# Performance work log

Measured on AMD Instinct MI355X. Metric: run time of the kernel, lower is better.

Reference implementation:

```python
import jax, jax.numpy as jnp
import numpy as np

EMBED_DIM = 256
MIN_SCALE = 0.5
BASE = 100.0
NDIM = 3
EPS = 1e-5


def basis_norm(psi, w):
    # w: [B, N] float weights; reduce over token dim (-2)
    norm_sq = jnp.sum(w[..., None] * (psi * psi), axis=-2, keepdims=True)
    return psi / jnp.sqrt(norm_sq + EPS)


def rotary(f, coords, lift):
    # lift: [D//2, 3]; phase: [B, N, D//2]
    phase = coords @ lift.T
    c, s = jnp.cos(phase), jnp.sin(phase)
    f1, f2 = jnp.split(f, 2, axis=-1)
    return jnp.concatenate([f1 * c - f2 * s, f1 * s + f2 * c], axis=-1)


def setup_inputs() -> dict:
    key = jax.random.key(0)
    ks = jax.random.split(key, 12)
    B, N, D = 4, 8192, EMBED_DIM
    phi = jax.random.normal(ks[0], (B, N, D), dtype=jnp.float32)
    coords = jax.random.normal(ks[1], (B, N, NDIM), dtype=jnp.float32)
    weights = jax.random.uniform(ks[2], (B, N), dtype=jnp.float32)
    scale = 1.0 / np.sqrt(D)
    Wq = jax.random.normal(ks[3], (D, D), dtype=jnp.float32) * scale
    bq = jnp.zeros((D,), dtype=jnp.float32)
    Wk = jax.random.normal(ks[4], (D, D), dtype=jnp.float32) * scale
    bk = jax.random.normal(ks[5], (D,), dtype=jnp.float32) * 0.01
    Wv = jax.random.normal(ks[6], (D, D), dtype=jnp.float32) * scale
    bv = jax.random.normal(ks[7], (D,), dtype=jnp.float32) * 0.01
    Wo = jax.random.normal(ks[8], (D, D), dtype=jnp.float32) * scale
    bo = jnp.zeros((D,), dtype=jnp.float32)
    # rotary lift init: k_norms * random unit vecs
    half = D // 2
    scales = BASE ** (-2.0 * np.arange(half) / D)
    k_norms = (2.0 * np.pi / MIN_SCALE) * scales  # [half]
    u = np.asarray(jax.random.normal(ks[9], (half, NDIM)))
    u = u / np.linalg.norm(u, axis=-1, keepdims=True)
    lift = jnp.asarray(k_norms[:, None] * u, dtype=jnp.float32)  # [half, 3]
    return {"phi": phi, "coords": coords, "weights": weights,
            "Wq": Wq, "bq": bq, "Wk": Wk, "bk": bk, "Wv": Wv, "bv": bv,
            "Wo": Wo, "bo": bo, "lift": lift}


def reference(phi, coords, weights, Wq, bq, Wk, bk, Wv, bv, Wo, bo, lift):
    q = phi @ Wq.T + bq
    k = basis_norm(phi @ Wk.T + bk, weights)
    v = basis_norm(phi @ Wv.T + bv, weights)
    q = rotary(q, coords, lift)
    k = rotary(k, coords, lift)
    k = k * weights[..., None]  # float-weights branch
    kv = jnp.einsum('bnd,bne->bde', k, v)   # [B, D, D]
    out = jnp.einsum('bnd,bde->bne', q, kv)  # [B, N, D]
    return out @ Wo.T + bo
```

## Files before the change

### kernel.cpp

```cpp
#include <hip/hip_runtime.h>
#include <hip/hip_bf16.h>
#include <stdint.h>

#define DEV __device__ __forceinline__

typedef short short8 __attribute__((ext_vector_type(8)));
typedef float floatx4 __attribute__((ext_vector_type(4)));

constexpr int D = 256;
constexpr int NTOK = 8192;
constexpr int MTOT = 4 * NTOK;

DEV void gl_lds16(const void* g, void* l) {
  __builtin_amdgcn_global_load_lds(
      (const __attribute__((address_space(1))) void*)g,
      (__attribute__((address_space(3))) void*)l, 16, 0, 0);
}

DEV float bflo(uint32_t u) { return __uint_as_float(u << 16); }
DEV float bfhi(uint32_t u) { return __uint_as_float(u & 0xffff0000u); }
DEV uint32_t packbf(float a, float b) {
  uint16_t xa = __builtin_bit_cast(uint16_t, __float2bfloat16(a));
  uint16_t xb = __builtin_bit_cast(uint16_t, __float2bfloat16(b));
  return (uint32_t)xa | ((uint32_t)xb << 16);
}

constexpr int PHI_E = MTOT * D;
constexpr int W_E = D * D;

__global__ __launch_bounds__(256) void convert(
    const float* __restrict__ phi, const float* __restrict__ Wq,
    const float* __restrict__ Wk, const float* __restrict__ Wv,
    const float* __restrict__ Wo,
    uint2* __restrict__ dst, float2* __restrict__ nszero) {
  if (blockIdx.x == 0) {
    const float2 z = {0.f, 0.f};
#pragma unroll
    for (int k = 0; k < 4; k++) nszero[k * 256 + threadIdx.x] = z;
  }
  const int idx4 = blockIdx.x * 256 + threadIdx.x;
  const int e0 = idx4 * 4;
  float4 v;
  if (e0 < PHI_E) {
    v = ((const float4*)phi)[idx4];
  } else {
    const int r = e0 - PHI_E;
    const int m = r >> 16;
    const int q = (r & 65535) >> 2;
    const float4* src = (m == 0) ? (const float4*)Wq : (m == 1) ? (const float4*)Wk
                      : (m == 2) ? (const float4*)Wv : (const float4*)Wo;
    v = src[q];
  }
  uint2 o;
  o.x = packbf(v.x, v.y);
  o.y = packbf(v.z, v.w);
  dst[idx4] = o;
}

__global__ __launch_bounds__(256, 4) void gemm_qkv(
    const __hip_bfloat16* __restrict__ phi,
    const __hip_bfloat16* __restrict__ W16,
    const float* __restrict__ bq, const float* __restrict__ bk, const float* __restrict__ bv,
    const float* __restrict__ coords, const float* __restrict__ wts,
    const float* __restrict__ lift,
    __hip_bfloat16* __restrict__ Qb, __hip_bfloat16* __restrict__ Kb,
    __hip_bfloat16* __restrict__ Vb, float* __restrict__ nsk, float* __restrict__ nsv) {
  __shared__ __align__(16) char As[8192];
  __shared__ __align__(16) char Bs[8192];
  const int t = threadIdx.x, lane = t & 63, wid = t >> 6;
  const int wm = (wid & 1) * 64;
  const int wn = (wid >> 1) * 32;
  const int l16 = lane & 15, q4 = lane >> 4;
  const int bid = blockIdx.x;
  const int g = (bid & 7) * 192 + (bid >> 3);
  const int sub = g % 6;
  const int mat = sub >> 1;
  const int nc0 = (sub & 1) * 64;
  const int m0 = (g / 6) * 128;
  const __hip_bfloat16* W = W16 + (size_t)mat * W_E;
  const float* bias = (mat == 0) ? bq : (mat == 1) ? bk : bv;
  __hip_bfloat16* Out = (mat == 0) ? Qb : (mat == 1) ? Kb : Vb;

  floatx4 acc[4][4] = {};

  const int srow = wid * 16 + (lane >> 2);
  const int skoff = (lane & 3) * 8;
  const __hip_bfloat16* gA = phi + (size_t)(m0 + srow) * D + skoff;
  const __hip_bfloat16* gB = W + (size_t)(nc0 + srow) * D + skoff;
  char* lA = As + srow * 64 + skoff * 2;
  char* lB = Bs + srow * 64 + skoff * 2;

  for (int kt = 0; kt < 256; kt += 32) {
    gl_lds16(gA + kt, lA);
    gl_lds16(gA + kt + 64 * D, lA + 4096);
    gl_lds16(gB + kt, lB);
    gl_lds16(gB + kt + 128 * D, lB + 4096);
    __syncthreads();
    short8 af[4], bf4[4];
#pragma unroll
    for (int i = 0; i < 4; i++)
      af[i] = *(const short8*)(As + (wm + i * 16 + l16) * 64 + q4 * 16);
#pragma unroll
    for (int j = 0; j < 4; j++) {
      const int brow = (j >> 1) * 64 + wn + (j & 1) * 16 + l16;
      bf4[j] = *(const short8*)(Bs + brow * 64 + q4 * 16);
    }
#pragma unroll
    for (int i = 0; i < 4; i++)
#pragma unroll
      for (int j = 0; j < 4; j++)
        acc[i][j] = __builtin_amdgcn_mfma_f32_16x16x32_bf16(af[i], bf4[j], acc[i][j], 0, 0, 0);
    __syncthreads();
  }

  float bcol[4];
#pragma unroll
  for (int j = 0; j < 4; j++)
    bcol[j] = bias[nc0 + wn + (j & 1) * 16 + (j >> 1) * 128 + l16];

  if (mat == 0) {
    float lx[2], ly[2], lz[2];
#pragma unroll
    for (int jj = 0; jj < 2; jj++) {
      const int c = nc0 + wn + jj * 16 + l16;
      lx[jj] = lift[c * 3 + 0]; ly[jj] = lift[c * 3 + 1]; lz[jj] = lift[c * 3 + 2];
    }
#pragma unroll
    for (int i = 0; i < 4; i++) {
#pragma unroll
      for (int r = 0; r < 4; r++) {
        const int row = m0 + wm + i * 16 + q4 * 4 + r;
        const float cx = coords[row * 3 + 0];
        const float cy = coords[row * 3 + 1];
        const float cz = coords[row * 3 + 2];
#pragma unroll
        for (int jj = 0; jj < 2; jj++) {
          const int c = nc0 + wn + jj * 16 + l16;
          const float p = cx * lx[jj] + cy * ly[jj] + cz * lz[jj];
          float s, cs;
          __sincosf(p, &s, &cs);
          const float f1 = acc[i][jj][r] + bcol[jj];
          const float f2 = acc[i][jj + 2][r] + bcol[jj + 2];
          Out[(size_t)row * D + c]       = __float2bfloat16(f1 * cs - f2 * s);
          Out[(size_t)row * D + c + 128] = __float2bfloat16(f1 * s + f2 * cs);
        }
      }
    }
  } else {
    const int b = m0 >> 13;
    float* ns = (mat == 1) ? nsk : nsv;
    float colsum[4] = {};
#pragma unroll
    for (int i = 0; i < 4; i++) {
#pragma unroll
      for (int r = 0; r < 4; r++) {
        const int row = m0 + wm + i * 16 + q4 * 4 + r;
        const float w = wts[row];
#pragma unroll
        for (int j = 0; j < 4; j++) {
          const int col = nc0 + wn + (j & 1) * 16 + (j >> 1) * 128 + l16;
          const float psi = acc[i][j][r] + bcol[j];
          Out[(size_t)row * D + col] = __float2bfloat16(psi);
          colsum[j] += w * psi * psi;
        }
      }
    }
#pragma unroll
    for (int j = 0; j < 4; j++) {
      float s = colsum[j];
      s += __shfl_xor(s, 16);
      s += __shfl_xor(s, 32);
      if (q4 == 0) {
        const int col = nc0 + wn + (j & 1) * 16 + (j >> 1) * 128 + l16;
        atomicAdd(&ns[b * D + col], s);
      }
    }
  }
}

__global__ __launch_bounds__(256, 2) void gemm_tn(
    const __hip_bfloat16* __restrict__ Kwb, const __hip_bfloat16* __restrict__ Vb,
    __hip_bfloat16* __restrict__ part, const float* __restrict__ coords,
    const float* __restrict__ wts, const float* __restrict__ lift,
    const float* __restrict__ nsk) {
  __shared__ __align__(16) char Asm[128 * 80];
  __shared__ __align__(16) char Bsm[128 * 80];
  const int t = threadIdx.x, lane = t & 63, wid = t >> 6;
  const int wm = (wid & 1) * 64, wn = (wid >> 1) * 64;
  const int l16 = lane & 15, q4 = lane >> 4;
  const int bid = blockIdx.x;
  const int g = (bid & 7) * 64 + (bid >> 3);
  const int ed = g & 3, rest = g >> 2;
  const int chunk = rest & 31, b = rest >> 5;
  const int d0 = (ed >> 1) * 128, e0 = (ed & 1) * 128;
  const uint32_t* A32 = (const uint32_t*)Kwb;
  const uint32_t* B32 = (const uint32_t*)Vb;
  const int s_np = (((t & 3) | ((t >> 6) << 2)) ^ ((t >> 4) & 3));
  const int s_e2lo = (t >> 2) & 15;
  float ikA[4], ikB[4], ikC[4], ikD[4];
  float lxa[4], lya[4], lza[4], lxb[4], lyb[4], lzb[4];
#pragma unroll
  for (int r = 0; r < 4; r++) {
    const int cl = 2 * (s_e2lo + r * 16);
    ikA[r] = rsqrtf(nsk[b * D + cl] + 1e-5f);
    ikB[r] = rsqrtf(nsk[b * D + cl + 1] + 1e-5f);
    ikC[r] = rsqrtf(nsk[b * D + cl + 128] + 1e-5f);
    ikD[r] = rsqrtf(nsk[b * D + cl + 129] + 1e-5f);
    lxa[r] = lift[cl * 3 + 0]; lya[r] = lift[cl * 3 + 1]; lza[r] = lift[cl * 3 + 2];
    lxb[r] = lift[cl * 3 + 3]; lyb[r] = lift[cl * 3 + 4]; lzb[r] = lift[cl * 3 + 5];
  }
  floatx4 acc[4][4] = {};
  for (int nt = 0; nt < 256; nt += 32) {
    const int nbase = chunk * 256 + nt;
    const size_t gt0 = (size_t)b * NTOK + nbase + 2 * s_np;
    const size_t tokbase = gt0 * 128;
    const float cx0 = coords[gt0 * 3 + 0], cy0 = coords[gt0 * 3 + 1], cz0 = coords[gt0 * 3 + 2];
    const float cx1 = coords[gt0 * 3 + 3], cy1 = coords[gt0 * 3 + 4], cz1 = coords[gt0 * 3 + 5];
    const float w0 = wts[gt0], w1 = wts[gt0 + 1];
#pragma unroll
    for (int r = 0; r < 4; r++) {
      const int e2 = s_e2lo + r * 16;
      const int dwA = (d0 >> 1) + e2;
      {
        const uint32_t a0 = A32[tokbase + dwA];
        const uint32_t a1 = A32[tokbase + 128 + dwA];
        const uint32_t p0 = A32[tokbase + (dwA ^ 64)];
        const uint32_t p1 = A32[tokbase + 128 + (dwA ^ 64)];
        float s00, c00, s01, c01, s10, c10, s11, c11;
        __sincosf(cx0 * lxa[r] + cy0 * lya[r] + cz0 * lza[r], &s00, &c00);
        __sincosf(cx0 * lxb[r] + cy0 * lyb[r] + cz0 * lzb[r], &s01, &c01);
        __sincosf(cx1 * lxa[r] + cy1 * lya[r] + cz1 * lza[r], &s10, &c10);
        __sincosf(cx1 * lxb[r] + cy1 * lyb[r] + cz1 * lzb[r], &s11, &c11);
        float oT0a, oT0b, oT1a, oT1b;
        if (d0 == 0) {
          oT0a = (bflo(a0) * ikA[r] * c00 - bflo(p0) * ikC[r] * s00) * w0;
          oT0b = (bfhi(a0) * ikB[r] * c01 - bfhi(p0) * ikD[r] * s01) * w0;
          oT1a = (bflo(a1) * ikA[r] * c10 - bflo(p1) * ikC[r] * s10) * w1;
          oT1b = (bfhi(a1) * ikB[r] * c11 - bfhi(p1) * ikD[r] * s11) * w1;
        } else {
          oT0a = (bflo(p0) * ikA[r] * s00 + bflo(a0) * ikC[r] * c00) * w0;
          oT0b = (bfhi(p0) * ikB[r] * s01 + bfhi(a0) * ikD[r] * c01) * w0;
          oT1a = (bflo(p1) * ikA[r] * s10 + bflo(a1) * ikC[r] * c10) * w1;
          oT1b = (bfhi(p1) * ikB[r] * s11 + bfhi(a1) * ikD[r] * c11) * w1;
        }
        *(uint32_t*)(Asm + (2 * e2) * 80 + 4 * s_np)     = packbf(oT0a, oT1a);
        *(uint32_t*)(Asm + (2 * e2 + 1) * 80 + 4 * s_np) = packbf(oT0b, oT1b);
      }
      {
        const uint32_t b0 = B32[tokbase + (e0 >> 1) + e2];
        const uint32_t b1 = B32[tokbase + 128 + (e0 >> 1) + e2];
        *(uint32_t*)(Bsm + (2 * e2) * 80 + 4 * s_np)     = (b0 & 0xffffu) | (b1 << 16);
        *(uint32_t*)(Bsm + (2 * e2 + 1) * 80 + 4 * s_np) = (b0 >> 16) | (b1 & 0xffff0000u);
      }
    }
    __syncthreads();
    short8 af[4], bf8[4];
#pragma unroll
    for (int i = 0; i < 4; i++) {
      af[i]  = *(const short8*)(Asm + (wm + i * 16 + l16) * 80 + q4 * 16);
      bf8[i] = *(const short8*)(Bsm + (wn + i * 16 + l16) * 80 + q4 * 16);
    }
#pragma unroll
    for (int i = 0; i < 4; i++)
#pragma unroll
      for (int j = 0; j < 4; j++)
        acc[i][j] = __builtin_amdgcn_mfma_f32_16x16x32_bf16(af[i], bf8[j], acc[i][j], 0, 0, 0);
    __syncthreads();
  }
  __hip_bfloat16* pt = part + (((size_t)(chunk * 4 + b)) << 16);
#pragma unroll
  for (int i = 0; i < 4; i++) {
#pragma unroll
    for (int r = 0; r < 4; r++) {
      const int rg = d0 + wm + i * 16 + q4 * 4 + r;
#pragma unroll
      for (int j = 0; j < 4; j++) {
        const int cg = e0 + wn + j * 16 + l16;
        pt[rg * 256 + cg] = __float2bfloat16(acc[i][j][r]);
      }
    }
  }
}

__global__ __launch_bounds__(256) void reduce_kvt(const uint32_t* __restrict__ part,
                                                  uint32_t* __restrict__ Ps,
                                                  const float* __restrict__ nsv) {
  const int flat2 = blockIdx.x * 256 + threadIdx.x;
  const int b = flat2 >> 15;
  const int off = flat2 & 32767;
  const int es = (off & 127) * 2;
  float sx = 0, sy = 0;
#pragma unroll
  for (int c = 0; c < 32; c++) {
    const uint32_t u = part[(((size_t)(c * 4 + b)) << 15) + off];
    sx += bflo(u); sy += bfhi(u);
  }
  const float iv0 = rsqrtf(nsv[b * D + es] + 1e-5f);
  const float iv1 = rsqrtf(nsv[b * D + es + 1] + 1e-5f);
  Ps[flat2] = packbf(sx * iv0, sy * iv1);
}

__global__ __launch_bounds__(256, 2) void gemm_mt(
    const __hip_bfloat16* __restrict__ Wo16, const __hip_bfloat16* __restrict__ Ps,
    __hip_bfloat16* __restrict__ MT) {
  __shared__ __align__(16) char As[8192];
  __shared__ __align__(16) char Bs[8192];
  const int t = threadIdx.x, lane = t & 63, wid = t >> 6;
  const int wm = (wid & 1) * 64, wn = (wid >> 1) * 64;
  const int l16 = lane & 15, q4 = lane >> 4;
  const int m0 = blockIdx.x * 128, n0 = blockIdx.y * 128, b = blockIdx.z;
  const __hip_bfloat16* Bm = Ps + ((size_t)b << 16);
  floatx4 acc[4][4] = {};
  const int srow = wid * 16 + (lane >> 2);
  const int skoff = (lane & 3) * 8;
  const __hip_bfloat16* gA = Wo16 + (size_t)(m0 + srow) * D + skoff;
  const __hip_bfloat16* gB = Bm + (size_t)(n0 + srow) * D + skoff;
  char* lA = As + srow * 64 + skoff * 2;
  char* lB = Bs + srow * 64 + skoff * 2;
  for (int kt = 0; kt < 256; kt += 32) {
    gl_lds16(gA + kt, lA);
    gl_lds16(gA + kt + 64 * D, lA + 4096);
    gl_lds16(gB + kt, lB);
    gl_lds16(gB + kt + 64 * D, lB + 4096);
    __syncthreads();
    short8 af[4], bf8[4];
#pragma unroll
    for (int i = 0; i < 4; i++) {
      af[i]  = *(const short8*)(As + (wm + i * 16 + l16) * 64 + q4 * 16);
      bf8[i] = *(const short8*)(Bs + (wn + i * 16 + l16) * 64 + q4 * 16);
    }
#pragma unroll
    for (int i = 0; i < 4; i++)
#pragma unroll
      for (int j = 0; j < 4; j++)
        acc[i][j] = __builtin_amdgcn_mfma_f32_16x16x32_bf16(af[i], bf8[j], acc[i][j], 0, 0, 0);
    __syncthreads();
  }
  __hip_bfloat16* Ob = MT + ((size_t)b << 16);
#pragma unroll
  for (int j = 0; j < 4; j++) {
    const int colg = n0 + wn + j * 16 + l16;
#pragma unroll
    for (int i = 0; i < 4; i++) {
      const int rowg = m0 + wm + i * 16 + q4 * 4;
#pragma unroll
      for (int r = 0; r < 4; r++)
        Ob[(size_t)(rowg + r) * D + colg] = __float2bfloat16(acc[i][j][r]);
    }
  }
}

__global__ __launch_bounds__(256, 2) void gemm_out(
    const __hip_bfloat16* __restrict__ A, const __hip_bfloat16* __restrict__ Pm,
    const float* __restrict__ bo, float* __restrict__ Og) {
  __shared__ __align__(16) char As[8192];
  __shared__ __align__(16) char Bs[8192];
  const int t = threadIdx.x, lane = t & 63, wid = t >> 6;
  const int wm = (wid & 1) * 64, wn = (wid >> 1) * 64;
  const int l16 = lane & 15, q4 = lane >> 4;
  const int m0 = blockIdx.x * 128, n0 = blockIdx.y * 128;
  const int b = m0 >> 13;
  const __hip_bfloat16* W = Pm + ((size_t)b << 16);
  floatx4 acc[4][4] = {};
  const int srow = wid * 16 + (lane >> 2);
  const int skoff = (lane & 3) * 8;
  const __hip_bfloat16* gA = A + (size_t)(m0 + srow) * D + skoff;
  const __hip_bfloat16* gB = W + (size_t)(n0 + srow) * D + skoff;
  char* lA = As + srow * 64 + skoff * 2;
  char* lB = Bs + srow * 64 + skoff * 2;
  for (int kt = 0; kt < 256; kt += 32) {
    gl_lds16(gA + kt, lA);
    gl_lds16(gA + kt + 64 * D, lA + 4096);
    gl_lds16(gB + kt, lB);
    gl_lds16(gB + kt + 64 * D, lB + 4096);
    __syncthreads();
    short8 af[4], bf8[4];
#pragma unroll
    for (int i = 0; i < 4; i++) {
      af[i]  = *(const short8*)(As + (wm + i * 16 + l16) * 64 + q4 * 16);
      bf8[i] = *(const short8*)(Bs + (wn + i * 16 + l16) * 64 + q4 * 16);
    }
#pragma unroll
    for (int i = 0; i < 4; i++)
#pragma unroll
      for (int j = 0; j < 4; j++)
        acc[i][j] = __builtin_amdgcn_mfma_f32_16x16x32_bf16(af[i], bf8[j], acc[i][j], 0, 0, 0);
    __syncthreads();
  }
#pragma unroll
  for (int j = 0; j < 4; j++) {
    const int colg = n0 + wn + j * 16 + l16;
    const float bb = bo[colg];
#pragma unroll
    for (int i = 0; i < 4; i++) {
      const int rowg = m0 + wm + i * 16 + q4 * 4;
#pragma unroll
      for (int r = 0; r < 4; r++)
        Og[(size_t)(rowg + r) * D + colg] = acc[i][j][r] + bb;
    }
  }
}

extern "C" void kernel_launch(void* const* d_in, const int* in_sizes, int n_in,
                              void* d_out, int out_size, void* d_ws, size_t ws_size,
                              hipStream_t stream) {
  const float* phi    = (const float*)d_in[0];
  const float* coords = (const float*)d_in[1];
  const float* wts    = (const float*)d_in[2];
  const float* bq     = (const float*)d_in[4];
  const float* bk     = (const float*)d_in[6];
  const float* bv     = (const float*)d_in[8];
  const float* Wo     = (const float*)d_in[9];
  const float* bo     = (const float*)d_in[10];
  const float* lift   = (const float*)d_in[11];

  char* ws = (char*)d_ws;
  __hip_bfloat16* phi16 = (__hip_bfloat16*)ws;
  __hip_bfloat16* W16   = (__hip_bfloat16*)(ws + 16777216);
  const size_t QOFF = 17301504;
  const size_t SZ = (size_t)MTOT * D * 2;
  __hip_bfloat16* Qb = (__hip_bfloat16*)(ws + QOFF);
  __hip_bfloat16* Kb = (__hip_bfloat16*)(ws + QOFF + SZ);
  __hip_bfloat16* Vb = (__hip_bfloat16*)(ws + QOFF + 2 * SZ);
  const size_t NOFF = QOFF + 3 * SZ;
  float* nsk = (float*)(ws + NOFF);
  float* nsv = (float*)(ws + NOFF + 4096);
  __hip_bfloat16* part = (__hip_bfloat16*)(ws + NOFF + 8192);
  __hip_bfloat16* Ps   = (__hip_bfloat16*)(ws + NOFF + 8192 + 16777216);
  __hip_bfloat16* MT   = (__hip_bfloat16*)(ws + NOFF + 8192 + 16777216 + 524288);

  convert<<<8448, 256, 0, stream>>>(phi, (const float*)d_in[3], (const float*)d_in[5],
                                    (const float*)d_in[7], Wo,
                                    (uint2*)ws, (float2*)(ws + NOFF));
  gemm_qkv<<<1536, 256, 0, stream>>>(phi16, W16, bq, bk, bv, coords, wts, lift,
                                     Qb, Kb, Vb, nsk, nsv);
  gemm_tn<<<512, 256, 0, stream>>>(Kb, Vb, part, coords, wts, lift, nsk);
  reduce_kvt<<<512, 256, 0, stream>>>((const uint32_t*)part, (uint32_t*)Ps, nsv);
  gemm_mt<<<dim3(2, 2, 4), 256, 0, stream>>>(W16 + 3 * W_E, Ps, MT);
  gemm_out<<<dim3(256, 2), 256, 0, stream>>>(Qb, MT, bo, (float*)d_out);
}
```

Before: 174.4 us.

## Replace split-K partial buffer and reduce kernel with fp32 atomics into KV accumulator

The TN GEMM now accumulates its per-chunk KV partial sums straight into a zeroed fp32 buffer with atomicAdd, instead of writing bf16 partials that a separate reduce kernel sums. The V-norm scaling and bf16 packing move into the gemm_mt B-tile load, and the convert kernel zeroes the accumulator. This removes one kernel launch and the 16MB partial write and read. In exchange there are 32-way atomic contentions per element and a scalar (non-async) B load path in gemm_mt.

Measured after the change: 192.9 us. 1.11x slower.

```diff
diff --git a/kernel.cpp b/kernel.cpp
--- a/kernel.cpp
+++ b/kernel.cpp
@@ -6,6 +6,7 @@
 
 typedef short short8 __attribute__((ext_vector_type(8)));
 typedef float floatx4 __attribute__((ext_vector_type(4)));
+typedef uint32_t uint32x4 __attribute__((ext_vector_type(4)));
 
 constexpr int D = 256;
 constexpr int NTOK = 8192;
@@ -32,11 +33,15 @@
     const float* __restrict__ phi, const float* __restrict__ Wq,
     const float* __restrict__ Wk, const float* __restrict__ Wv,
     const float* __restrict__ Wo,
-    uint2* __restrict__ dst, float2* __restrict__ nszero) {
+    uint2* __restrict__ dst, float2* __restrict__ nszero, float4* __restrict__ psz) {
   if (blockIdx.x == 0) {
     const float2 z = {0.f, 0.f};
 #pragma unroll
     for (int k = 0; k < 4; k++) nszero[k * 256 + threadIdx.x] = z;
+  }
+  if (blockIdx.x < 256) {
+    const float4 z4 = {0.f, 0.f, 0.f, 0.f};
+    psz[blockIdx.x * 256 + threadIdx.x] = z4;
   }
   const int idx4 = blockIdx.x * 256 + threadIdx.x;
   const int e0 = idx4 * 4;
@@ -180,7 +185,7 @@
 
 __global__ __launch_bounds__(256, 2) void gemm_tn(
     const __hip_bfloat16* __restrict__ Kwb, const __hip_bfloat16* __restrict__ Vb,
-    __hip_bfloat16* __restrict__ part, const float* __restrict__ coords,
+    float* __restrict__ Psacc, const float* __restrict__ coords,
     const float* __restrict__ wts, const float* __restrict__ lift,
     const float* __restrict__ nsk) {
   __shared__ __align__(16) char Asm[128 * 80];
@@ -267,7 +272,7 @@
         acc[i][j] = __builtin_amdgcn_mfma_f32_16x16x32_bf16(af[i], bf8[j], acc[i][j], 0, 0, 0);
     __syncthreads();
   }
-  __hip_bfloat16* pt = part + (((size_t)(chunk * 4 + b)) << 16);
+  float* pa = Psacc + ((size_t)b << 16);
 #pragma unroll
   for (int i = 0; i < 4; i++) {
 #pragma unroll
@@ -276,52 +281,53 @@
 #pragma unroll
       for (int j = 0; j < 4; j++) {
         const int cg = e0 + wn + j * 16 + l16;
-        pt[rg * 256 + cg] = __float2bfloat16(acc[i][j][r]);
-      }
-    }
-  }
-}
-
-__global__ __launch_bounds__(256) void reduce_kvt(const uint32_t* __restrict__ part,
-                                                  uint32_t* __restrict__ Ps,
-                                                  const float* __restrict__ nsv) {
-  const int flat2 = blockIdx.x * 256 + threadIdx.x;
-  const int b = flat2 >> 15;
-  const int off = flat2 & 32767;
-  const int es = (off & 127) * 2;
-  float sx = 0, sy = 0;
-#pragma unroll
-  for (int c = 0; c < 32; c++) {
-    const uint32_t u = part[(((size_t)(c * 4 + b)) << 15) + off];
-    sx += bflo(u); sy += bfhi(u);
-  }
-  const float iv0 = rsqrtf(nsv[b * D + es] + 1e-5f);
-  const float iv1 = rsqrtf(nsv[b * D + es + 1] + 1e-5f);
-  Ps[flat2] = packbf(sx * iv0, sy * iv1);
+        atomicAdd(&pa[rg * 256 + cg], acc[i][j][r]);
+      }
+    }
+  }
 }
 
 __global__ __launch_bounds__(256, 2) void gemm_mt(
-    const __hip_bfloat16* __restrict__ Wo16, const __hip_bfloat16* __restrict__ Ps,
-    __hip_bfloat16* __restrict__ MT) {
+    const __hip_bfloat16* __restrict__ Wo16, const float* __restrict__ Psacc,
+    const float* __restrict__ nsv, __hip_bfloat16* __restrict__ MT) {
   __shared__ __align__(16) char As[8192];
   __shared__ __align__(16) char Bs[8192];
+  __shared__ __align__(16) float isv[256];
   const int t = threadIdx.x, lane = t & 63, wid = t >> 6;
   const int wm = (wid & 1) * 64, wn = (wid >> 1) * 64;
   const int l16 = lane & 15, q4 = lane >> 4;
   const int m0 = blockIdx.x * 128, n0 = blockIdx.y * 128, b = blockIdx.z;
-  const __hip_bfloat16* Bm = Ps + ((size_t)b << 16);
+  isv[t] = rsqrtf(nsv[b * D + t] + 1e-5f);
+  __syncthreads();
+  const float* Bm = Psacc + ((size_t)b << 16);
   floatx4 acc[4][4] = {};
   const int srow = wid * 16 + (lane >> 2);
   const int skoff = (lane & 3) * 8;
   const __hip_bfloat16* gA = Wo16 + (size_t)(m0 + srow) * D + skoff;
-  const __hip_bfloat16* gB = Bm + (size_t)(n0 + srow) * D + skoff;
+  const float* gB0 = Bm + (size_t)(n0 + srow) * D + skoff;
+  const float* gB1 = Bm + (size_t)(n0 + srow + 64) * D + skoff;
   char* lA = As + srow * 64 + skoff * 2;
   char* lB = Bs + srow * 64 + skoff * 2;
   for (int kt = 0; kt < 256; kt += 32) {
     gl_lds16(gA + kt, lA);
     gl_lds16(gA + kt + 64 * D, lA + 4096);
-    gl_lds16(gB + kt, lB);
-    gl_lds16(gB + kt + 64 * D, lB + 4096);
+    const float4 w0 = *(const float4*)(gB0 + kt);
+    const float4 w1 = *(const float4*)(gB0 + kt + 4);
+    const float4 w2 = *(const float4*)(gB1 + kt);
+    const float4 w3 = *(const float4*)(gB1 + kt + 4);
+    const float4 i0 = *(const float4*)(&isv[kt + skoff]);
+    const float4 i1 = *(const float4*)(&isv[kt + skoff + 4]);
+    uint32x4 p0, p1;
+    p0[0] = packbf(w0.x * i0.x, w0.y * i0.y);
+    p0[1] = packbf(w0.z * i0.z, w0.w * i0.w);
+    p0[2] = packbf(w1.x * i1.x, w1.y * i1.y);
+    p0[3] = packbf(w1.z * i1.z, w1.w * i1.w);
+    p1[0] = packbf(w2.x * i0.x, w2.y * i0.y);
+    p1[1] = packbf(w2.z * i0.z, w2.w * i0.w);
+    p1[2] = packbf(w3.x * i1.x, w3.y * i1.y);
+    p1[3] = packbf(w3.z * i1.z, w3.w * i1.w);
+    *(uint32x4*)lB = p0;
+    *(uint32x4*)(lB + 4096) = p1;
     __syncthreads();
     short8 af[4], bf8[4];
 #pragma unroll
@@ -425,17 +431,15 @@
   const size_t NOFF = QOFF + 3 * SZ;
   float* nsk = (float*)(ws + NOFF);
   float* nsv = (float*)(ws + NOFF + 4096);
-  __hip_bfloat16* part = (__hip_bfloat16*)(ws + NOFF + 8192);
-  __hip_bfloat16* Ps   = (__hip_bfloat16*)(ws + NOFF + 8192 + 16777216);
-  __hip_bfloat16* MT   = (__hip_bfloat16*)(ws + NOFF + 8192 + 16777216 + 524288);
+  float* Psacc = (float*)(ws + NOFF + 8192);
+  __hip_bfloat16* MT = (__hip_bfloat16*)(ws + NOFF + 8192 + 1048576);
 
   convert<<<8448, 256, 0, stream>>>(phi, (const float*)d_in[3], (const float*)d_in[5],
                                     (const float*)d_in[7], Wo,
-                                    (uint2*)ws, (float2*)(ws + NOFF));
+                                    (uint2*)ws, (float2*)(ws + NOFF), (float4*)Psacc);
   gemm_qkv<<<1536, 256, 0, stream>>>(phi16, W16, bq, bk, bv, coords, wts, lift,
                                      Qb, Kb, Vb, nsk, nsv);
-  gemm_tn<<<512, 256, 0, stream>>>(Kb, Vb, part, coords, wts, lift, nsk);
-  reduce_kvt<<<512, 256, 0, stream>>>((const uint32_t*)part, (uint32_t*)Ps, nsv);
-  gemm_mt<<<dim3(2, 2, 4), 256, 0, stream>>>(W16 + 3 * W_E, Ps, MT);
+  gemm_tn<<<512, 256, 0, stream>>>(Kb, Vb, Psacc, coords, wts, lift, nsk);
+  gemm_mt<<<dim3(2, 2, 4), 256, 0, stream>>>(W16 + 3 * W_E, Psacc, nsv, MT);
   gemm_out<<<dim3(256, 2), 256, 0, stream>>>(Qb, MT, bo, (float*)d_out);
 }
```
